# Performance work log

Hardware: AMD Instinct MI355X
Metric: run time of the kernel (lower is better)

The kernel has to match this reference:

```python
import jax, jax.numpy as jnp
import numpy as np

B, Q, S, D, H = 4, 1024, 4096, 256, 8
HD = D // H
NEG = -1000000000.0


def setup_inputs() -> dict:
    key = jax.random.key(0)
    ks = jax.random.split(key, 12)
    s = 1.0 / np.sqrt(D)
    inp = {
        "query": jax.random.normal(ks[0], (B, Q, D), jnp.float32),
        "key": jax.random.normal(ks[1], (B, S, D), jnp.float32),
        "value": jax.random.normal(ks[2], (B, S, D), jnp.float32),
        "attention_mask": jax.random.randint(ks[3], (B, Q, S), 0, 2) > 0,
        # nn.Linear weights stored as [out, in]; we apply x @ W.T + b
        "wq": jax.random.uniform(ks[4], (D, D), jnp.float32, -s, s),
        "bq": jnp.zeros((D,), jnp.float32),
        "wk": jax.random.uniform(ks[5], (D, D), jnp.float32, -s, s),
        "bk": jnp.zeros((D,), jnp.float32),
        "wv": jax.random.uniform(ks[6], (D, D), jnp.float32, -s, s),
        "bv": jnp.zeros((D,), jnp.float32),
        "wo": jax.random.uniform(ks[7], (D, D), jnp.float32, -s, s),
        "bo": jnp.zeros((D,), jnp.float32),
        "ln_g": jnp.ones((D,), jnp.float32),
        "ln_b": jnp.zeros((D,), jnp.float32),
    }
    return inp


def _layernorm(x, g, b, eps=1e-5):
    mu = jnp.mean(x, axis=-1, keepdims=True)
    var = jnp.var(x, axis=-1, keepdims=True)
    return (x - mu) * jax.lax.rsqrt(var + eps) * g + b


def reference(query, key, value, attention_mask, wq, bq, wk, bk, wv, bv, wo, bo, ln_g, ln_b):
    residual = query
    x = _layernorm(query, ln_g, ln_b)
    q = x @ wq.T + bq                       # [B,Q,D]
    k = key @ wk.T + bk                     # [B,S,D]
    v = value @ wv.T + bv                   # [B,S,D]
    q = q.reshape(B, Q, H, HD).transpose(0, 2, 1, 3)   # [B,H,Q,HD]
    k = k.reshape(B, S, H, HD).transpose(0, 2, 1, 3)   # [B,H,S,HD]
    v = v.reshape(B, S, H, HD).transpose(0, 2, 1, 3)   # [B,H,S,HD]
    scale = HD ** -0.5
    scores = jnp.einsum("bhqd,bhsd->bhqs", q, k) * scale   # [B,H,Q,S]
    scores = jnp.where(attention_mask[:, None, :, :], scores, NEG)
    attn = jax.nn.softmax(scores, axis=-1)
    # dropout is identity in eval/inference mode
    out = jnp.einsum("bhqs,bhsd->bhqd", attn, v)            # [B,H,Q,HD]
    out = out.transpose(0, 2, 1, 3).reshape(B, Q, D)
    out = out @ wo.T + bo
    return out + residual
```

## Files before the change

### kernel.cpp

```cpp
#include <hip/hip_runtime.h>
#include <cmath>

#define BQ 4
#define QL 1024
#define SL 4096
#define DM 256
#define NH 8
#define HD 32
#define NROWS 32768
#define NSPLIT 4
#define SEG (SL / NSPLIT)

typedef __attribute__((ext_vector_type(8))) short short8;
typedef __attribute__((ext_vector_type(4))) short short4v;
typedef __attribute__((ext_vector_type(4))) float f32x4;
typedef __attribute__((ext_vector_type(4))) unsigned int uint4v;
typedef __attribute__((ext_vector_type(2))) unsigned int uint2v;
typedef unsigned long long u64;

#define MFMA16(a, b, c) __builtin_amdgcn_mfma_f32_16x16x32_bf16((a), (b), (c), 0, 0, 0)

__device__ __forceinline__ short f2bf(float f) {
  union { float f; unsigned int u; } x; x.f = f;
  unsigned int r = x.u + 0x7FFFu + ((x.u >> 16) & 1u);
  return (short)(r >> 16);
}
__device__ __forceinline__ unsigned int fu(float f) {
  union { float f; unsigned int u; } x; x.f = f; return x.u;
}
__device__ __forceinline__ unsigned int cvtpk(float lo, float hi) {
  unsigned int r;
  asm("v_cvt_pk_bf16_f32 %0, %1, %2" : "=v"(r) : "v"(lo), "v"(hi));
  return r;
}

__global__ __launch_bounds__(256) void wcvt_kernel(const float* __restrict__ wq,
                                                   const float* __restrict__ wk,
                                                   const float* __restrict__ wv,
                                                   const float* __restrict__ wo,
                                                   const uint4v* __restrict__ mask4,
                                                   unsigned int* __restrict__ flags,
                                                   short* __restrict__ w16) {
  if (blockIdx.x == 0) {
    __shared__ int fA, fB;
    if (threadIdx.x == 0) { fA = 0; fB = 0; }
    __syncthreads();
    unsigned int a = 0, bb = 0;
#pragma unroll
    for (int i = 0; i < 16; ++i) {
      uint4v v = mask4[threadIdx.x * 16 + i];
#pragma unroll
      for (int e = 0; e < 4; ++e) {
        a |= (v[e] & 0xFEFEFEFEu);
        bb |= (v[e] & 0xFFFFFF00u);
      }
    }
    if (a) atomicOr(&fA, 1);
    if (bb) atomicOr(&fB, 1);
    __syncthreads();
    if (threadIdx.x == 0) flags[0] = (fA || !fB) ? 4u : 1u;
  }
  const int i = blockIdx.x * 256 + threadIdx.x;
  const float* src;
  short* dst;
  if (i < 8192)       { src = wq + i * 8;            dst = w16 + i * 8; }
  else if (i < 16384) { src = wk + (i - 8192) * 8;   dst = w16 + 65536 + (i - 8192) * 8; }
  else if (i < 24576) { src = wv + (i - 16384) * 8;  dst = w16 + 131072 + (i - 16384) * 8; }
  else                { src = wo + (i - 24576) * 8;  dst = w16 + 196608 + (i - 24576) * 8; }
  f32x4 a0 = *(const f32x4*)src;
  f32x4 a1 = *(const f32x4*)(src + 4);
  uint4v o = {cvtpk(a0[0], a0[1]), cvtpk(a0[2], a0[3]),
              cvtpk(a1[0], a1[1]), cvtpk(a1[2], a1[3])};
  *(uint4v*)dst = o;
}

__global__ __launch_bounds__(256) void masknln_kernel(const void* __restrict__ mask,
                                                      const unsigned int* __restrict__ flags,
                                                      u64* __restrict__ MB,
                                                      const float* __restrict__ x,
                                                      const float* __restrict__ gw,
                                                      const float* __restrict__ bw,
                                                      short* __restrict__ xout) {
  const int i = blockIdx.x * 256 + threadIdx.x;
  u64 bits = 0;
  if (flags[0] == 4u) {
    const uint4v* src = (const uint4v*)mask + (size_t)i * 16;
#pragma unroll
    for (int c = 0; c < 16; ++c) {
      uint4v v = src[c];
      unsigned int nib = 0;
#pragma unroll
      for (int e = 0; e < 4; ++e) nib |= (v[e] != 0u ? 1u : 0u) << e;
      bits |= (u64)nib << ((c & 3) * 16 + (c >> 2) * 4);
    }
  } else {
    const uint4v* src = (const uint4v*)mask + (size_t)i * 4;
#pragma unroll
    for (int c = 0; c < 4; ++c) {
      uint4v v = src[c];
#pragma unroll
      for (int e4 = 0; e4 < 4; ++e4) {
        const unsigned int u = v[e4];
        unsigned int nib = 0;
        nib |= (u & 0x000000FFu) ? 1u : 0u;
        nib |= (u & 0x0000FF00u) ? 2u : 0u;
        nib |= (u & 0x00FF0000u) ? 4u : 0u;
        nib |= (u & 0xFF000000u) ? 8u : 0u;
        bits |= (u64)nib << (e4 * 16 + c * 4);
      }
    }
  }
  MB[i] = bits;
  const int lane = threadIdx.x & 63;
  const int row = blockIdx.x * 4 + (threadIdx.x >> 6);
  const float* xr = x + (size_t)row * DM;
  f32x4 v = *(const f32x4*)(xr + lane * 4);
  float s = v[0] + v[1] + v[2] + v[3];
  float s2 = v[0]*v[0] + v[1]*v[1] + v[2]*v[2] + v[3]*v[3];
#pragma unroll
  for (int m = 1; m < 64; m <<= 1) { s += __shfl_xor(s, m); s2 += __shfl_xor(s2, m); }
  const float mu = s * (1.0f / DM);
  const float var = s2 * (1.0f / DM) - mu * mu;
  const float inv = rsqrtf(var + 1e-5f);
  f32x4 gv = *(const f32x4*)(gw + lane * 4);
  f32x4 bv = *(const f32x4*)(bw + lane * 4);
  float y0 = (v[0] - mu) * inv * gv[0] + bv[0];
  float y1 = (v[1] - mu) * inv * gv[1] + bv[1];
  float y2 = (v[2] - mu) * inv * gv[2] + bv[2];
  float y3 = (v[3] - mu) * inv * gv[3] + bv[3];
  uint2v o = {cvtpk(y0, y1), cvtpk(y2, y3)};
  *(uint2v*)(xout + (size_t)row * DM + lane * 4) = o;
}

template <int EPI>
__global__ __launch_bounds__(256) void gemm_bt(const float* __restrict__ Af,
                                               const short* __restrict__ W16,
                                               const float* __restrict__ bias,
                                               void* __restrict__ outp) {
  __shared__ __align__(16) short As[2][64][72];
  __shared__ __align__(16) short Bs[2][64][72];
  const int t = threadIdx.x;
  const int lane = t & 63, w = t >> 6;
  const int wm = w >> 1, wn = w & 1;
  const int g = lane >> 4, lr = lane & 15, gsh = g * 4;
  const int bid = blockIdx.x;
  const int x = bid & 7, j = bid >> 3;
  const int mt8 = gridDim.x >> 5;
  const int m0 = (x * mt8 + (j >> 2)) * 64;
  const int n0 = (j & 3) * 64;
  const int row = (t * 2) >> 3, cc0 = (t * 2) & 7;
  f32x4 acc[2][2] = {};

  f32x4 apf[2][2];
  short8 bn[2];
#pragma unroll
  for (int c = 0; c < 2; ++c) {
    const float* s = Af + (size_t)(m0 + row) * DM + (cc0 + c) * 8;
    apf[c][0] = *(const f32x4*)s;
    apf[c][1] = *(const f32x4*)(s + 4);
    bn[c] = *(const short8*)(W16 + (size_t)(n0 + row) * DM + (cc0 + c) * 8);
  }
  for (int k0 = 0; k0 < 4; ++k0) {
    const int buf = k0 & 1;
#pragma unroll
    for (int c = 0; c < 2; ++c) {
      uint4v sv = {cvtpk(apf[c][0][0], apf[c][0][1]), cvtpk(apf[c][0][2], apf[c][0][3]),
                   cvtpk(apf[c][1][0], apf[c][1][1]), cvtpk(apf[c][1][2], apf[c][1][3])};
      *(uint4v*)&As[buf][row][(cc0 + c) * 8] = sv;
      *(short8*)&Bs[buf][row][(cc0 + c) * 8] = bn[c];
    }
    __syncthreads();
    if (k0 < 3) {
#pragma unroll
      for (int c = 0; c < 2; ++c) {
        const float* s = Af + (size_t)(m0 + row) * DM + (k0 + 1) * 64 + (cc0 + c) * 8;
        apf[c][0] = *(const f32x4*)s;
        apf[c][1] = *(const f32x4*)(s + 4);
        bn[c] = *(const short8*)(W16 + (size_t)(n0 + row) * DM + (k0 + 1) * 64 + (cc0 + c) * 8);
      }
    }
#pragma unroll
    for (int ks = 0; ks < 2; ++ks) {
      short8 af[2], bfr[2];
#pragma unroll
      for (int i = 0; i < 2; ++i) af[i] = *(const short8*)&As[buf][wm * 32 + i * 16 + lr][ks * 32 + g * 8];
#pragma unroll
      for (int jj = 0; jj < 2; ++jj) bfr[jj] = *(const short8*)&Bs[buf][wn * 32 + jj * 16 + lr][ks * 32 + g * 8];
#pragma unroll
      for (int i = 0; i < 2; ++i)
#pragma unroll
        for (int jj = 0; jj < 2; ++jj) acc[i][jj] = MFMA16(af[i], bfr[jj], acc[i][jj]);
    }
  }
  if (EPI == 1) {
#pragma unroll
    for (int i = 0; i < 2; ++i)
#pragma unroll
      for (int jj = 0; jj < 2; ++jj) {
        const int nl = wn * 32 + jj * 16 + lr;
        const float bv = bias[n0 + nl];
#pragma unroll
        for (int r = 0; r < 4; ++r)
          As[0][wm * 32 + i * 16 + gsh + r][nl] = f2bf(acc[i][jj][r] + bv);
      }
    __syncthreads();
#pragma unroll
    for (int c = 0; c < 2; ++c) {
      const int idx = t * 2 + c, dl = idx >> 3, ch = idx & 7;
      *(short8*)((short*)outp + (size_t)(m0 + dl) * DM + n0 + ch * 8) =
          *(const short8*)&As[0][dl][ch * 8];
    }
  } else {
#pragma unroll
    for (int i = 0; i < 2; ++i)
#pragma unroll
      for (int jj = 0; jj < 2; ++jj) {
        const int nl = wn * 32 + jj * 16 + lr;
        const float bv = bias[n0 + nl];
        uint2v pk2 = {cvtpk(acc[i][jj][0] + bv, acc[i][jj][1] + bv),
                      cvtpk(acc[i][jj][2] + bv, acc[i][jj][3] + bv)};
        *(uint2v*)&As[0][nl][wm * 32 + i * 16 + gsh] = pk2;
      }
    __syncthreads();
    const int bidx = m0 >> 12, sbase = m0 & (SL - 1);
#pragma unroll
    for (int c = 0; c < 2; ++c) {
      const int idx = t * 2 + c, dl = idx >> 3, ch = idx & 7;
      *(short8*)((short*)outp + ((size_t)bidx * DM + n0 + dl) * SL + sbase + ch * 8) =
          *(const short8*)&As[0][dl][ch * 8];
    }
  }
}

template <int EPI>
__global__ __launch_bounds__(256) void gemm32(const short* __restrict__ A16,
                                              const float* __restrict__ Op,
                                              const float* __restrict__ Lp,
                                              const short* __restrict__ W16,
                                              const float* __restrict__ bias,
                                              void* __restrict__ outp,
                                              const float* __restrict__ resid,
                                              float oscale) {
  __shared__ __align__(16) short As[2][32][72];
  __shared__ __align__(16) short Bs[2][32][72];
  const int t = threadIdx.x;
  const int lane = t & 63, w = t >> 6;
  const int wm = w >> 1, wn = w & 1;
  const int g = lane >> 4, lr = lane & 15, gsh = g * 4;
  const int bid = blockIdx.x;
  const int x = bid & 7, j = bid >> 3;
  const int m0 = (x * 16 + (j >> 3)) * 32;
  const int n0 = (j & 7) * 32;
  const int row = t >> 3, cc = t & 7;
  const int trow = m0 + row;
  f32x4 acc = {0.f, 0.f, 0.f, 0.f};

  short8 aval;
  short8 bval;
  auto produceA = [&](int k) -> short8 {
    if (EPI == 0) {
      return *(const short8*)(A16 + (size_t)trow * DM + k * 64 + cc * 8);
    } else {
      const int kcol = k * 64 + cc * 8;
      const int h = kcol >> 5, hd = kcol & 31;
      const size_t rid = ((size_t)((trow >> 10) * NH + h)) * QL + (trow & (QL - 1));
      float den = 0.0f;
      f32x4 o0 = {0.f, 0.f, 0.f, 0.f}, o1 = {0.f, 0.f, 0.f, 0.f};
#pragma unroll
      for (int i = 0; i < NSPLIT; ++i) {
        const size_t base = ((size_t)i * NROWS + rid) * 32 + hd;
        den += Lp[(size_t)i * NROWS + rid];
        const f32x4 pa = *(const f32x4*)(Op + base);
        const f32x4 pb = *(const f32x4*)(Op + base + 4);
#pragma unroll
        for (int e = 0; e < 4; ++e) { o0[e] += pa[e]; o1[e] += pb[e]; }
      }
      const float inv = __builtin_amdgcn_rcpf(den);
      union { uint4v u; short8 s; } pk;
      pk.u = uint4v{cvtpk(o0[0] * inv, o0[1] * inv), cvtpk(o0[2] * inv, o0[3] * inv),
                    cvtpk(o1[0] * inv, o1[1] * inv), cvtpk(o1[2] * inv, o1[3] * inv)};
      return pk.s;
    }
  };
  aval = produceA(0);
  bval = *(const short8*)(W16 + (size_t)(n0 + row) * DM + cc * 8);

  for (int k0 = 0; k0 < 4; ++k0) {
    const int buf = k0 & 1;
    *(short8*)&As[buf][row][cc * 8] = aval;
    *(short8*)&Bs[buf][row][cc * 8] = bval;
    __syncthreads();
    if (k0 < 3) {
      aval = produceA(k0 + 1);
      bval = *(const short8*)(W16 + (size_t)(n0 + row) * DM + (k0 + 1) * 64 + cc * 8);
    }
#pragma unroll
    for (int ks = 0; ks < 2; ++ks) {
      short8 af = *(const short8*)&As[buf][wm * 16 + lr][ks * 32 + g * 8];
      short8 bf = *(const short8*)&Bs[buf][wn * 16 + lr][ks * 32 + g * 8];
      acc = MFMA16(af, bf, acc);
    }
  }
  if (EPI == 0) {
    const int nl = wn * 16 + lr;
    const float bv = bias[n0 + nl];
#pragma unroll
    for (int r = 0; r < 4; ++r)
      As[0][wm * 16 + gsh + r][nl] = f2bf((acc[r] + bv) * oscale);
    __syncthreads();
    *(short4v*)((short*)outp + (size_t)trow * DM + n0 + (t & 7) * 4) =
        *(const short4v*)&As[0][row][(t & 7) * 4];
  } else {
#pragma unroll
    for (int r = 0; r < 4; ++r) {
      const int rr = m0 + wm * 16 + gsh + r;
      const int col = n0 + wn * 16 + lr;
      ((float*)outp)[(size_t)rr * DM + col] =
          acc[r] + bias[col] + resid[(size_t)rr * DM + col];
    }
  }
}

__global__ __launch_bounds__(256, 4) void attn_kernel(const short* __restrict__ qb,
                                                      const short* __restrict__ kb,
                                                      const short* __restrict__ vbT,
                                                      const unsigned short* __restrict__ MB,
                                                      float* __restrict__ Op,
                                                      float* __restrict__ Lp) {
  __shared__ __align__(16) short Ks[2][64][40];
  __shared__ __align__(16) short Vs[2][32][76];

  const int n_ = blockIdx.x;
  const int x_ = n_ & 7, j_ = n_ >> 3;
  const int grp = ((j_ >> 5) << 3) + x_;
  const int within = j_ & 31;
  const int q0 = (within & 7) * 128;
  const int split = within >> 3;
  const int h = grp & 7, b = grp >> 3;

  const int t = threadIdx.x;
  const int l = t & 63, w = t >> 6;
  const int g = l >> 4, lr = l & 15, gsh = g * 4;
  const int qbase = q0 + w * 32;
  const int srow = t >> 2, scc = t & 3;
  const int vd = t >> 3, vsc = t & 7;

  const short* Kp = kb + ((size_t)b * SL + split * SEG + srow) * DM + h * HD + scc * 8;
  const short* Vp = vbT + ((size_t)(b * NH + h) * HD + vd) * SL + split * SEG + vsc * 8;
  const unsigned short* MBp0 =
      MB + (((size_t)(b * QL) + qbase + lr) * 64 + split * (SEG / 64)) * 4 + g;
  const unsigned short* MBp1 = MBp0 + 16 * 64 * 4;

  const short8 qf0 =
      *(const short8*)(qb + ((size_t)(b * QL) + qbase + lr) * DM + h * HD + g * 8);
  const short8 qf1 =
      *(const short8*)(qb + ((size_t)(b * QL) + qbase + 16 + lr) * DM + h * HD + g * 8);

  const short ONE = (short)0x3F80;
  const short8 ONES = {ONE, ONE, ONE, ONE, ONE, ONE, ONE, ONE};
  f32x4 Ov0[2] = {}, Ov1[2] = {};
  f32x4 Ls0 = {0.f, 0.f, 0.f, 0.f}, Ls1 = {0.f, 0.f, 0.f, 0.f};

  short8 kreg[2], vreg[2];
  unsigned int mbA[2], mbB[2];
  kreg[0] = *(const short8*)Kp;
  vreg[0] = *(const short8*)Vp;
  mbA[0] = MBp0[0]; mbB[0] = MBp1[0];
  kreg[1] = *(const short8*)(Kp + (size_t)64 * DM);
  vreg[1] = *(const short8*)(Vp + 64);
  mbA[1] = MBp0[4]; mbB[1] = MBp1[4];

#pragma unroll 2
  for (int it = 0; it < SEG / 64; ++it) {
    const int buf = it & 1;
    *(short8*)&Ks[buf][srow][scc * 8] = kreg[buf];
    {
      short4v lo = {vreg[buf][0], vreg[buf][1], vreg[buf][2], vreg[buf][3]};
      short4v hi = {vreg[buf][4], vreg[buf][5], vreg[buf][6], vreg[buf][7]};
      *(short4v*)&Vs[buf][vd][vsc * 8] = lo;
      *(short4v*)&Vs[buf][vd][vsc * 8 + 4] = hi;
    }
    const unsigned int mb0 = mbA[buf], mb1 = mbB[buf];
    __syncthreads();
    if (it < SEG / 64 - 2) {
      kreg[buf] = *(const short8*)(Kp + (size_t)(it + 2) * 64 * DM);
      vreg[buf] = *(const short8*)(Vp + (it + 2) * 64);
      mbA[buf] = MBp0[(it + 2) * 4];
      mbB[buf] = MBp1[(it + 2) * 4];
    }

    const f32x4 z = {0.f, 0.f, 0.f, 0.f};
    f32x4 sc0[4], sc1[4];
#pragma unroll
    for (int f = 0; f < 4; ++f) {
      short8 kf = *(const short8*)&Ks[buf][f * 16 + lr][g * 8];
      sc0[f] = MFMA16(kf, qf0, z);
      sc1[f] = MFMA16(kf, qf1, z);
    }
#pragma unroll
    for (int ks = 0; ks < 2; ++ks) {
      unsigned int pk0[2][2], pk1[2][2];
#pragma unroll
      for (int fi = 0; fi < 2; ++fi) {
        const int f = 2 * ks + fi;
        unsigned int p0[4], p1[4];
#pragma unroll
        for (int r = 0; r < 4; ++r) {
          const unsigned int m0b = (unsigned int)(-(int)((mb0 >> (f * 4 + r)) & 1u));
          const unsigned int m1b = (unsigned int)(-(int)((mb1 >> (f * 4 + r)) & 1u));
          p0[r] = fu(__builtin_amdgcn_exp2f(sc0[f][r])) & m0b;
          p1[r] = fu(__builtin_amdgcn_exp2f(sc1[f][r])) & m1b;
        }
        pk0[fi][0] = __builtin_amdgcn_perm(p0[0], p0[1], 0x03020706u);
        pk0[fi][1] = __builtin_amdgcn_perm(p0[2], p0[3], 0x03020706u);
        pk1[fi][0] = __builtin_amdgcn_perm(p1[0], p1[1], 0x03020706u);
        pk1[fi][1] = __builtin_amdgcn_perm(p1[2], p1[3], 0x03020706u);
      }
      union { unsigned int u[4]; short8 v; } pa0, pa1;
      pa0.u[0] = pk0[0][0]; pa0.u[1] = pk0[0][1]; pa0.u[2] = pk0[1][0]; pa0.u[3] = pk0[1][1];
      pa1.u[0] = pk1[0][0]; pa1.u[1] = pk1[0][1]; pa1.u[2] = pk1[1][0]; pa1.u[3] = pk1[1][1];
      Ls0 = MFMA16(pa0.v, ONES, Ls0);
      Ls1 = MFMA16(pa1.v, ONES, Ls1);
#pragma unroll
      for (int n = 0; n < 2; ++n) {
        short4v va = *(const short4v*)&Vs[buf][n * 16 + lr][(2 * ks) * 16 + gsh];
        short4v vb2 = *(const short4v*)&Vs[buf][n * 16 + lr][(2 * ks + 1) * 16 + gsh];
        union { short4v h[2]; short8 v; } vf;
        vf.h[0] = va; vf.h[1] = vb2;
        Ov0[n] = MFMA16(pa0.v, vf.v, Ov0[n]);
        Ov1[n] = MFMA16(pa1.v, vf.v, Ov1[n]);
      }
    }
  }
  const int ridx = (b * NH + h) * QL + qbase;
  const size_t pb = (size_t)split * NROWS + ridx;
#pragma unroll
  for (int n = 0; n < 2; ++n)
#pragma unroll
    for (int r = 0; r < 4; ++r) {
      Op[(pb + gsh + r) * 32 + n * 16 + lr] = Ov0[n][r];
      Op[(pb + 16 + gsh + r) * 32 + n * 16 + lr] = Ov1[n][r];
    }
  if (lr == 0) {
#pragma unroll
    for (int r = 0; r < 4; ++r) {
      Lp[pb + gsh + r] = Ls0[r];
      Lp[pb + 16 + gsh + r] = Ls1[r];
    }
  }
}

extern "C" void kernel_launch(void* const* d_in, const int* in_sizes, int n_in,
                              void* d_out, int out_size, void* d_ws, size_t ws_size,
                              hipStream_t stream) {
  const float* query = (const float*)d_in[0];
  const float* key   = (const float*)d_in[1];
  const float* value = (const float*)d_in[2];
  const void*  mask  = d_in[3];
  const float* wq = (const float*)d_in[4];
  const float* bq = (const float*)d_in[5];
  const float* wk = (const float*)d_in[6];
  const float* bk = (const float*)d_in[7];
  const float* wv = (const float*)d_in[8];
  const float* bv = (const float*)d_in[9];
  const float* wo = (const float*)d_in[10];
  const float* bo = (const float*)d_in[11];
  const float* lng = (const float*)d_in[12];
  const float* lnb = (const float*)d_in[13];
  float* out = (float*)d_out;

  char* ws = (char*)d_ws;
  unsigned int* flags = (unsigned int*)ws;
  float* Lp  = (float*)(ws + (4u << 10));
  short* xln = (short*)(ws + (2u << 20));
  short* qb  = (short*)(ws + (4u << 20));
  short* kb  = (short*)(ws + (6u << 20));
  short* vbT = (short*)(ws + (14u << 20));
  u64*   mbt = (u64*)(ws + (22u << 20));
  short* w16 = (short*)(ws + (24u << 20));
  float* Op  = (float*)(ws + (25u << 20));

  const float qscale = (float)(1.4426950408889634 / sqrt((double)HD));

  wcvt_kernel<<<128, 256, 0, stream>>>(wq, wk, wv, wo, (const uint4v*)mask, flags, w16);
  masknln_kernel<<<1024, 256, 0, stream>>>(mask, flags, mbt, query, lng, lnb, xln);
  gemm32<0><<<1024, 256, 0, stream>>>(xln, nullptr, nullptr, w16, bq, qb, nullptr, qscale);
  gemm_bt<1><<<(BQ * SL / 64) * 4, 256, 0, stream>>>(key, w16 + 65536, bk, kb);
  gemm_bt<3><<<(BQ * SL / 64) * 4, 256, 0, stream>>>(value, w16 + 131072, bv, vbT);
  attn_kernel<<<1024, 256, 0, stream>>>(qb, kb, vbT, (const unsigned short*)mbt, Op, Lp);
  gemm32<2><<<1024, 256, 0, stream>>>(nullptr, Op, Lp, w16 + 196608, bo, out, query, 1.0f);
}
```

Measured before the change: 92.29 us.

## Load K/V fragments directly from global into registers, dropping LDS staging

The attention kernel no longer stages K and V tiles through double-buffered shared memory with a block-wide barrier. Each wave now loads its own MFMA operand fragments for K and transposed V straight from global memory into registers, and prefetches the next iteration's fragments and mask bits while computing the current one. This removes the LDS writes, the LDS reads and __syncthreads. In exchange, the four waves of a block each fetch the same K/V data, so global/L2 traffic rises, the V loads become narrower strided accesses, and the last iteration prefetches past the segment end, which can read beyond the buffer.

```diff
diff --git a/kernel.cpp b/kernel.cpp
--- a/kernel.cpp
+++ b/kernel.cpp
@@ -327,9 +327,6 @@
                                                       const unsigned short* __restrict__ MB,
                                                       float* __restrict__ Op,
                                                       float* __restrict__ Lp) {
-  __shared__ __align__(16) short Ks[2][64][40];
-  __shared__ __align__(16) short Vs[2][32][76];
-
   const int n_ = blockIdx.x;
   const int x_ = n_ & 7, j_ = n_ >> 3;
   const int grp = ((j_ >> 5) << 3) + x_;
@@ -342,11 +339,9 @@
   const int l = t & 63, w = t >> 6;
   const int g = l >> 4, lr = l & 15, gsh = g * 4;
   const int qbase = q0 + w * 32;
-  const int srow = t >> 2, scc = t & 3;
-  const int vd = t >> 3, vsc = t & 7;
-
-  const short* Kp = kb + ((size_t)b * SL + split * SEG + srow) * DM + h * HD + scc * 8;
-  const short* Vp = vbT + ((size_t)(b * NH + h) * HD + vd) * SL + split * SEG + vsc * 8;
+
+  const short* Kp = kb + ((size_t)b * SL + split * SEG + lr) * DM + h * HD + g * 8;
+  const short* Vp = vbT + ((size_t)(b * NH + h) * HD + lr) * SL + split * SEG + gsh;
   const unsigned short* MBp0 =
       MB + (((size_t)(b * QL) + qbase + lr) * 64 + split * (SEG / 64)) * 4 + g;
   const unsigned short* MBp1 = MBp0 + 16 * 64 * 4;
@@ -361,41 +356,34 @@
   f32x4 Ov0[2] = {}, Ov1[2] = {};
   f32x4 Ls0 = {0.f, 0.f, 0.f, 0.f}, Ls1 = {0.f, 0.f, 0.f, 0.f};
 
-  short8 kreg[2], vreg[2];
-  unsigned int mbA[2], mbB[2];
-  kreg[0] = *(const short8*)Kp;
-  vreg[0] = *(const short8*)Vp;
-  mbA[0] = MBp0[0]; mbB[0] = MBp1[0];
-  kreg[1] = *(const short8*)(Kp + (size_t)64 * DM);
-  vreg[1] = *(const short8*)(Vp + 64);
-  mbA[1] = MBp0[4]; mbB[1] = MBp1[4];
-
-#pragma unroll 2
+  short8 kf[4];
+  short4v vf[2][4];
+  unsigned int mb0, mb1;
+#pragma unroll
+  for (int f = 0; f < 4; ++f) kf[f] = *(const short8*)(Kp + (size_t)(f * 16) * DM);
+#pragma unroll
+  for (int n = 0; n < 2; ++n)
+#pragma unroll
+    for (int k2 = 0; k2 < 4; ++k2)
+      vf[n][k2] = *(const short4v*)(Vp + (size_t)n * 16 * SL + k2 * 16);
+  mb0 = MBp0[0];
+  mb1 = MBp1[0];
+
   for (int it = 0; it < SEG / 64; ++it) {
-    const int buf = it & 1;
-    *(short8*)&Ks[buf][srow][scc * 8] = kreg[buf];
-    {
-      short4v lo = {vreg[buf][0], vreg[buf][1], vreg[buf][2], vreg[buf][3]};
-      short4v hi = {vreg[buf][4], vreg[buf][5], vreg[buf][6], vreg[buf][7]};
-      *(short4v*)&Vs[buf][vd][vsc * 8] = lo;
-      *(short4v*)&Vs[buf][vd][vsc * 8 + 4] = hi;
-    }
-    const unsigned int mb0 = mbA[buf], mb1 = mbB[buf];
-    __syncthreads();
-    if (it < SEG / 64 - 2) {
-      kreg[buf] = *(const short8*)(Kp + (size_t)(it + 2) * 64 * DM);
-      vreg[buf] = *(const short8*)(Vp + (it + 2) * 64);
-      mbA[buf] = MBp0[(it + 2) * 4];
-      mbB[buf] = MBp1[(it + 2) * 4];
-    }
-
     const f32x4 z = {0.f, 0.f, 0.f, 0.f};
     f32x4 sc0[4], sc1[4];
 #pragma unroll
     for (int f = 0; f < 4; ++f) {
-      short8 kf = *(const short8*)&Ks[buf][f * 16 + lr][g * 8];
-      sc0[f] = MFMA16(kf, qf0, z);
-      sc1[f] = MFMA16(kf, qf1, z);
+      sc0[f] = MFMA16(kf[f], qf0, z);
+      sc1[f] = MFMA16(kf[f], qf1, z);
+    }
+    unsigned int mb0n, mb1n;
+    {
+      const short* Kn = Kp + (size_t)(it + 1) * 64 * DM;
+#pragma unroll
+      for (int f = 0; f < 4; ++f) kf[f] = *(const short8*)(Kn + (size_t)(f * 16) * DM);
+      mb0n = MBp0[(it + 1) * 4];
+      mb1n = MBp1[(it + 1) * 4];
     }
 #pragma unroll
     for (int ks = 0; ks < 2; ++ks) {
@@ -423,14 +411,23 @@
       Ls1 = MFMA16(pa1.v, ONES, Ls1);
 #pragma unroll
       for (int n = 0; n < 2; ++n) {
-        short4v va = *(const short4v*)&Vs[buf][n * 16 + lr][(2 * ks) * 16 + gsh];
-        short4v vb2 = *(const short4v*)&Vs[buf][n * 16 + lr][(2 * ks + 1) * 16 + gsh];
-        union { short4v h[2]; short8 v; } vf;
-        vf.h[0] = va; vf.h[1] = vb2;
-        Ov0[n] = MFMA16(pa0.v, vf.v, Ov0[n]);
-        Ov1[n] = MFMA16(pa1.v, vf.v, Ov1[n]);
-      }
-    }
+        union { short4v h[2]; short8 v; } vv;
+        vv.h[0] = vf[n][2 * ks];
+        vv.h[1] = vf[n][2 * ks + 1];
+        Ov0[n] = MFMA16(pa0.v, vv.v, Ov0[n]);
+        Ov1[n] = MFMA16(pa1.v, vv.v, Ov1[n]);
+      }
+    }
+    {
+      const short* Vn = Vp + (it + 1) * 64;
+#pragma unroll
+      for (int n = 0; n < 2; ++n)
+#pragma unroll
+        for (int k2 = 0; k2 < 4; ++k2)
+          vf[n][k2] = *(const short4v*)(Vn + (size_t)n * 16 * SL + k2 * 16);
+    }
+    mb0 = mb0n;
+    mb1 = mb1n;
   }
   const int ridx = (b * NH + h) * QL + qbase;
   const size_t pb = (size_t)split * NROWS + ridx;
```

Result: slower. 160.1 us (+73.4%).
